# Optimization experiments

Measured on AMD Instinct MI355X. Metric: run time of the kernel, lower is better.

Reference implementation:

```python
import jax, jax.numpy as jnp
import numpy as np

EPS = 1e-6  # torch F.normalize eps


def setup_inputs() -> dict:
    key = jax.random.key(0)
    ks = jax.random.split(key, 9)
    B, C, H, W = 2, 256, 64, 64
    nH, dk, dv = 4, 64, 64
    s = 0.05  # weight scale for numerical stability
    return {
        "x": jax.random.normal(ks[0], (B, C, H, W), jnp.float32),
        "Wq": jax.random.normal(ks[1], (nH, dk, C), jnp.float32) * s,
        "bq": jax.random.normal(ks[2], (nH, dk), jnp.float32) * s,
        "Wk": jax.random.normal(ks[3], (nH, dk, C), jnp.float32) * s,
        "bk": jax.random.normal(ks[4], (nH, dk), jnp.float32) * s,
        "Wv": jax.random.normal(ks[5], (nH, dv, C), jnp.float32) * s,
        "bv": jax.random.normal(ks[6], (nH, dv), jnp.float32) * s,
        "Wm": jax.random.normal(ks[7], (C, nH * dv), jnp.float32) * s,
        "bm": jax.random.normal(ks[8], (C,), jnp.float32) * s,
    }


def _l2norm(t):
    # torch F.normalize along channel dim (axis=2 here: [B,H,dk,L])
    n = jnp.sqrt(jnp.sum(t * t, axis=2, keepdims=True))
    return t / jnp.maximum(n, EPS)


def reference(x, Wq, bq, Wk, bk, Wv, bv, Wm, bm):
    B, C, H, W = x.shape
    nH = Wq.shape[0]
    L = H * W
    xf = x.reshape(B, C, L)  # 1x1 conv == channel matmul on flattened spatial
    # per-head projections: [B, nH, d, L]
    Q = jnp.einsum('bcl,hdc->bhdl', xf, Wq) + bq[None, :, :, None]
    K = jnp.einsum('bcl,hdc->bhdl', xf, Wk) + bk[None, :, :, None]
    V = jnp.einsum('bcl,hvc->bhvl', xf, Wv) + bv[None, :, :, None]
    Q = _l2norm(Q)
    K = _l2norm(K)
    # cosine-similarity scores A[b,h,i,j] = sum_d Q[b,h,d,i] K[b,h,d,j]
    A = jnp.einsum('bhdi,bhdj->bhij', Q, K)
    A = jax.nn.softmax(A, axis=-1)
    # R[b,h,v,i] = sum_j A[b,h,i,j] V[b,h,v,j]
    R = jnp.einsum('bhij,bhvj->bhvi', A, V)
    # concat heads along channels -> [B, nH*dv, L]
    Rc = R.reshape(B, nH * V.shape[2], L)
    out = jnp.einsum('bcl,oc->bol', Rc, Wm) + bm[None, :, None]
    out = out.reshape(B, C, H, W) + x  # residual
    return out
```

## Files before the change

### kernel.cpp

```cpp
#include <hip/hip_runtime.h>
#include <hip/hip_bf16.h>
#include <cstdint>
#include <cstddef>

typedef __bf16 bf16;
typedef bf16 bf16x8 __attribute__((ext_vector_type(8)));
typedef bf16 bf16x4 __attribute__((ext_vector_type(4)));
typedef bf16 bf16x2 __attribute__((ext_vector_type(2)));
typedef float f32x4 __attribute__((ext_vector_type(4)));

#define MFMA16(A, B, Cc) __builtin_amdgcn_mfma_f32_16x16x32_bf16((A), (B), (Cc), 0, 0, 0)
#define GLD16(g, l)                                                          \
  __builtin_amdgcn_global_load_lds(                                          \
      (const __attribute__((address_space(1))) void*)(g),                    \
      (__attribute__((address_space(3))) void*)(l), 16, 0, 0)

static constexpr int L   = 4096;
static constexpr int CH  = 256;
static constexpr int NH  = 4;

static constexpr size_t OFF_WALL = 0;
static constexpr size_t OFF_WMB  = 393216;
static constexpr size_t OFF_BALL = 524288;
static constexpr size_t OFF_XT   = 528384;
static constexpr size_t OFF_QT   = 4722688;
static constexpr size_t OFF_KT   = 8916992;
static constexpr size_t OFF_VD   = 13111296;
static constexpr size_t OFF_RP1  = 17305600;
static constexpr size_t OFF_RP2  = 21499904;
static constexpr size_t OFF_RP3  = 25694208;
static constexpr size_t OFF_DP4  = 29888512;
static constexpr size_t OFF_DP2  = 21499904;
static constexpr size_t NEED4    = 30412800;

__global__ __launch_bounds__(256) void k_wcvt(
    const float* __restrict__ Wq, const float* __restrict__ Wk,
    const float* __restrict__ Wv, const float* __restrict__ bq,
    const float* __restrict__ bk, const float* __restrict__ bv,
    const float* __restrict__ Wm, bf16* __restrict__ Wall,
    float* __restrict__ ball, bf16* __restrict__ Wmb) {
  int id = blockIdx.x * 256 + threadIdx.x;
  if (id < 65536)        Wall[id] = (bf16)Wq[id];
  else if (id < 131072)  Wall[id] = (bf16)Wk[id - 65536];
  else if (id < 196608)  Wall[id] = (bf16)Wv[id - 131072];
  else if (id < 262144)  Wmb[id - 196608] = (bf16)Wm[id - 196608];
  else if (id < 262912) {
    int k = id - 262144;
    ball[k] = (k < 256) ? bq[k] : (k < 512) ? bk[k - 256] : bv[k - 512];
  }
}

__global__ __launch_bounds__(256) void k_tx(const float* __restrict__ x,
                                            bf16* __restrict__ xT) {
  __shared__ float t[32][33];
  const int b = blockIdx.z, c0 = blockIdx.y * 32, l0 = blockIdx.x * 32;
  const int tx = threadIdx.x, ty = threadIdx.y;
  #pragma unroll
  for (int i = 0; i < 4; ++i) {
    int c = c0 + ty + 8 * i;
    t[ty + 8 * i][tx] = x[((size_t)b * CH + c) * L + l0 + tx];
  }
  __syncthreads();
  #pragma unroll
  for (int i = 0; i < 4; ++i) {
    int l = l0 + ty + 8 * i;
    xT[((size_t)b * L + l) * CH + c0 + tx] = (bf16)t[tx][ty + 8 * i];
  }
}

__global__ __launch_bounds__(256) void k_proj(
    const bf16* __restrict__ Wall, const float* __restrict__ ball,
    const bf16* __restrict__ xT, bf16* __restrict__ Qt,
    bf16* __restrict__ Kt, bf16* __restrict__ Vd) {
  const int b = blockIdx.z, strip = blockIdx.y, lt = blockIdx.x;
  const int w = threadIdx.x >> 6;
  const int lane = threadIdx.x & 63;
  const int lo = lane & 15, g = lane >> 4;
  const int l0 = lt * 256 + w * 64;

  const bf16* wbase = Wall + (size_t)strip * 64 * CH;
  const bf16* xbase = xT + (size_t)b * L * CH;

  f32x4 acc[4][4];
  #pragma unroll
  for (int m = 0; m < 4; ++m)
    #pragma unroll
    for (int n = 0; n < 4; ++n) acc[m][n] = (f32x4){0.f, 0.f, 0.f, 0.f};

  #pragma unroll
  for (int kc = 0; kc < 8; ++kc) {
    bf16x8 aw[4], bx[4];
    #pragma unroll
    for (int m = 0; m < 4; ++m)
      aw[m] = *(const bf16x8*)(wbase + (size_t)(16 * m + lo) * CH + kc * 32 + g * 8);
    #pragma unroll
    for (int n = 0; n < 4; ++n)
      bx[n] = *(const bf16x8*)(xbase + (size_t)(l0 + 16 * n + lo) * CH + kc * 32 + g * 8);
    #pragma unroll
    for (int m = 0; m < 4; ++m)
      #pragma unroll
      for (int n = 0; n < 4; ++n) acc[m][n] = MFMA16(aw[m], bx[n], acc[m][n]);
  }

  #pragma unroll
  for (int m = 0; m < 4; ++m)
    #pragma unroll
    for (int r = 0; r < 4; ++r) {
      float bias = ball[strip * 64 + 16 * m + 4 * g + r];
      #pragma unroll
      for (int n = 0; n < 4; ++n) acc[m][n][r] += bias;
    }

  if (strip < 8) {
    #pragma unroll
    for (int n = 0; n < 4; ++n) {
      float ss = 0.f;
      #pragma unroll
      for (int m = 0; m < 4; ++m)
        #pragma unroll
        for (int r = 0; r < 4; ++r) ss += acc[m][n][r] * acc[m][n][r];
      ss += __shfl_xor(ss, 16);
      ss += __shfl_xor(ss, 32);
      float sc = 1.f / fmaxf(sqrtf(ss), 1e-6f);
      #pragma unroll
      for (int m = 0; m < 4; ++m)
        #pragma unroll
        for (int r = 0; r < 4; ++r) acc[m][n][r] *= sc;
    }
    bf16* dst = (strip < 4) ? Qt : Kt;
    const int h = strip & 3;
    #pragma unroll
    for (int n = 0; n < 4; ++n) {
      const int l = l0 + 16 * n + lo;
      #pragma unroll
      for (int m = 0; m < 4; ++m) {
        size_t base = ((size_t)(b * NH + h) * L + l) * 64 + 16 * m + 4 * g;
        bf16x2 v01, v23;
        v01[0] = (bf16)acc[m][n][0]; v01[1] = (bf16)acc[m][n][1];
        v23[0] = (bf16)acc[m][n][2]; v23[1] = (bf16)acc[m][n][3];
        *(bf16x2*)(dst + base)     = v01;
        *(bf16x2*)(dst + base + 2) = v23;
      }
    }
  } else {
    const int h = strip - 8;
    #pragma unroll
    for (int m = 0; m < 4; ++m)
      #pragma unroll
      for (int r = 0; r < 4; ++r) {
        const int d = 16 * m + 4 * g + r;
        #pragma unroll
        for (int n = 0; n < 4; ++n) {
          const int l = l0 + 16 * n + lo;
          Vd[((size_t)(b * NH + h) * 64 + d) * L + l] = (bf16)acc[m][n][r];
        }
      }
  }
}


#define STAGE(bb, j0)                                                          \
  {                                                                            \
    const char* gk0 = kbase + (size_t)((j0) + sr) * 128 + scS;                 \
    const char* gk1 = kbase + (size_t)((j0) + 32 + sr) * 128 + scS;            \
    const char* gv0 = vbase + (size_t)sr * 8192 + (size_t)(j0) * 2 + scS;      \
    const char* gv1 = vbase + (size_t)(32 + sr) * 8192 + (size_t)(j0) * 2 + scS; \
    GLD16(gk0, kbuf[bb] + w * 1024 + lane * 16);                               \
    GLD16(gk1, kbuf[bb] + 4096 + w * 1024 + lane * 16);                        \
    GLD16(gv0, vbuf[bb] + w * 1024 + lane * 16);                               \
    GLD16(gv1, vbuf[bb] + 4096 + w * 1024 + lane * 16);                        \
  }

#define COMPUTE(bb)                                                            \
  {                                                                            \
    const char* kb = kbuf[bb];                                                 \
    const char* vb = vbuf[bb];                                                 \
    _Pragma("unroll") for (int t = 0; t < 4; ++t) {                            \
      bf16x8 kf0 = *(const bf16x8*)(kb + (16 * t + lo) * 128 + ((16 * g) ^ sw)); \
      bf16x8 kf1 = *(const bf16x8*)(kb + (16 * t + lo) * 128 + ((64 + 16 * g) ^ sw)); \
      _Pragma("unroll") for (int m = 0; m < 4; ++m) {                          \
        f32x4 z = (f32x4){0.f, 0.f, 0.f, 0.f};                                 \
        z = MFMA16(kf0, qf[m][0], z);                                          \
        z = MFMA16(kf1, qf[m][1], z);                                          \
        float p0 = __expf(z[0]), p1 = __expf(z[1]);                            \
        float p2 = __expf(z[2]), p3 = __expf(z[3]);                            \
        den[m] += (p0 + p1) + (p2 + p3);                                       \
        bf16x4 pk;                                                             \
        pk[0] = (bf16)p0; pk[1] = (bf16)p1; pk[2] = (bf16)p2; pk[3] = (bf16)p3; \
        *(bf16x4*)(pbw + (16 * m + lo) * 128 + ((32 * t + 8 * g) ^ sw)) = pk;  \
      }                                                                        \
    }                                                                          \
    bf16x8 pa[4][2];                                                           \
    _Pragma("unroll") for (int m = 0; m < 4; ++m)                              \
      _Pragma("unroll") for (int s = 0; s < 2; ++s)                            \
        pa[m][s] = *(const bf16x8*)(pbw + (16 * m + lo) * 128 + ((64 * s + 16 * g) ^ sw)); \
    _Pragma("unroll") for (int n = 0; n < 4; ++n) {                            \
      bf16x8 vf0 = *(const bf16x8*)(vb + (16 * n + lo) * 128 + ((16 * g) ^ sw)); \
      bf16x8 vf1 = *(const bf16x8*)(vb + (16 * n + lo) * 128 + ((64 + 16 * g) ^ sw)); \
      _Pragma("unroll") for (int m = 0; m < 4; ++m) {                          \
        racc[m][n] = MFMA16(pa[m][0], vf0, racc[m][n]);                        \
        racc[m][n] = MFMA16(pa[m][1], vf1, racc[m][n]);                        \
      }                                                                        \
    }                                                                          \
  }

template <int JS>
__global__ __launch_bounds__(256, 2) void k_attn(
    const bf16* __restrict__ Qt, const bf16* __restrict__ Kt,
    const bf16* __restrict__ Vd, bf16* __restrict__ R0,
    bf16* __restrict__ R1, bf16* __restrict__ R2, bf16* __restrict__ R3,
    float* __restrict__ D0, float* __restrict__ D1,
    float* __restrict__ D2, float* __restrict__ D3) {
  const int id = blockIdx.x;
  const int bh = id & 7;
  const int qt = (id >> 3) & 15;
  const int js = id >> 7;
  const int tid = threadIdx.x;
  const int w = tid >> 6;
  const int lane = tid & 63;
  const int lo = lane & 15, g = lane >> 4;
  const int sw = (lo & 7) << 4;
  const int i0 = qt * 256 + w * 64;

  __shared__ __align__(16) char kbuf[2][8192];
  __shared__ __align__(16) char vbuf[2][8192];
  __shared__ __align__(16) char pbuf[4][8192];
  char* pbw = pbuf[w];

  const char* kbase = (const char*)(Kt + (size_t)bh * L * 64);
  const char* vbase = (const char*)(Vd + (size_t)bh * 64 * L);

  const int sr = tid >> 3;
  const int sc = (tid & 7) * 16;
  const int scS = sc ^ ((sr & 7) << 4);

  const bf16* qb = Qt + ((size_t)bh * L + i0) * 64;
  bf16x8 qf[4][2];
  #pragma unroll
  for (int m = 0; m < 4; ++m)
    #pragma unroll
    for (int s = 0; s < 2; ++s)
      qf[m][s] = *(const bf16x8*)(qb + (size_t)(16 * m + lo) * 64 + 32 * s + 8 * g);

  f32x4 racc[4][4];
  #pragma unroll
  for (int m = 0; m < 4; ++m)
    #pragma unroll
    for (int n = 0; n < 4; ++n) racc[m][n] = (f32x4){0.f, 0.f, 0.f, 0.f};
  float den[4] = {0.f, 0.f, 0.f, 0.f};

  const int jbeg = js * (L / JS);
  const int nt = (L / JS) / 64;

  STAGE(0, jbeg)
  __syncthreads();
  for (int it = 0; it < nt; ++it) {
    const int bb = it & 1;
    if (it + 1 < nt) STAGE(bb ^ 1, jbeg + (it + 1) * 64)
    COMPUTE(bb)
    __syncthreads();
  }

  #pragma unroll
  for (int m = 0; m < 4; ++m) {
    den[m] += __shfl_xor(den[m], 16);
    den[m] += __shfl_xor(den[m], 32);
  }

  bf16* rp = (js == 0) ? R0 : (js == 1) ? R1 : (js == 2) ? R2 : R3;
  float* dp = (js == 0) ? D0 : (js == 1) ? D1 : (js == 2) ? D2 : D3;

  if (g == 0) {
    #pragma unroll
    for (int m = 0; m < 4; ++m)
      dp[(size_t)bh * L + i0 + 16 * m + lo] = den[m];
  }
  #pragma unroll
  for (int m = 0; m < 4; ++m)
    #pragma unroll
    for (int n = 0; n < 4; ++n)
      #pragma unroll
      for (int r = 0; r < 4; ++r) {
        const int q = 16 * m + 4 * g + r;
        rp[((size_t)bh * L + i0 + q) * 64 + 16 * n + lo] = (bf16)racc[m][n][r];
      }
}

template <int JS>
__global__ __launch_bounds__(256) void k_comb(
    const bf16* __restrict__ R0, const bf16* __restrict__ R1,
    const bf16* __restrict__ R2, const bf16* __restrict__ R3,
    const float* __restrict__ D0, const float* __restrict__ D1,
    const float* __restrict__ D2, const float* __restrict__ D3,
    bf16* __restrict__ Rt) {
  const int tid = blockIdx.x * 256 + threadIdx.x;
  const int e8 = tid * 8;
  const int d8 = e8 & 63;
  const int l = (e8 >> 6) & (L - 1);
  const int bh = e8 >> 18;
  const size_t di = (size_t)bh * L + l;
  float den = D0[di] + D1[di];
  if (JS == 4) den += D2[di] + D3[di];
  const float inv = 1.0f / den;
  bf16x8 a0 = *(const bf16x8*)(R0 + e8);
  bf16x8 a1 = *(const bf16x8*)(R1 + e8);
  bf16x8 o;
  if (JS == 4) {
    bf16x8 a2 = *(const bf16x8*)(R2 + e8);
    bf16x8 a3 = *(const bf16x8*)(R3 + e8);
    #pragma unroll
    for (int e = 0; e < 8; ++e)
      o[e] = (bf16)((((float)a0[e] + (float)a1[e]) + ((float)a2[e] + (float)a3[e])) * inv);
  } else {
    #pragma unroll
    for (int e = 0; e < 8; ++e)
      o[e] = (bf16)(((float)a0[e] + (float)a1[e]) * inv);
  }
  *(bf16x8*)(Rt + ((size_t)(bh >> 2) * L + l) * CH + (bh & 3) * 64 + d8) = o;
}

__global__ __launch_bounds__(256) void k_out(
    const bf16* __restrict__ Wmb, const bf16* __restrict__ Rt,
    const float* __restrict__ x, const float* __restrict__ bm,
    float* __restrict__ out) {
  const int b = blockIdx.y, lt = blockIdx.x;
  const int w = threadIdx.x >> 6;
  const int lane = threadIdx.x & 63;
  const int lo = lane & 15, g = lane >> 4;
  const int o0 = w * 64, l0 = lt * 64;

  f32x4 acc[4][4];
  #pragma unroll
  for (int m = 0; m < 4; ++m)
    #pragma unroll
    for (int n = 0; n < 4; ++n) acc[m][n] = (f32x4){0.f, 0.f, 0.f, 0.f};

  #pragma unroll
  for (int kc = 0; kc < 8; ++kc) {
    bf16x8 aw[4], bx[4];
    #pragma unroll
    for (int m = 0; m < 4; ++m)
      aw[m] = *(const bf16x8*)(Wmb + (size_t)(o0 + 16 * m + lo) * CH + kc * 32 + g * 8);
    #pragma unroll
    for (int n = 0; n < 4; ++n)
      bx[n] = *(const bf16x8*)(Rt + ((size_t)b * L + l0 + 16 * n + lo) * CH + kc * 32 + g * 8);
    #pragma unroll
    for (int m = 0; m < 4; ++m)
      #pragma unroll
      for (int n = 0; n < 4; ++n) acc[m][n] = MFMA16(aw[m], bx[n], acc[m][n]);
  }

  #pragma unroll
  for (int m = 0; m < 4; ++m)
    #pragma unroll
    for (int r = 0; r < 4; ++r) {
      const int o = o0 + 16 * m + 4 * g + r;
      const float bias = bm[o];
      #pragma unroll
      for (int n = 0; n < 4; ++n) {
        const int l = l0 + 16 * n + lo;
        size_t idx = ((size_t)b * CH + o) * (size_t)L + l;
        out[idx] = acc[m][n][r] + bias + x[idx];
      }
    }
}

extern "C" void kernel_launch(void* const* d_in, const int* in_sizes, int n_in,
                              void* d_out, int out_size, void* d_ws, size_t ws_size,
                              hipStream_t stream) {
  const float* x  = (const float*)d_in[0];
  const float* Wq = (const float*)d_in[1];
  const float* bq = (const float*)d_in[2];
  const float* Wk = (const float*)d_in[3];
  const float* bk = (const float*)d_in[4];
  const float* Wv = (const float*)d_in[5];
  const float* bv = (const float*)d_in[6];
  const float* Wm = (const float*)d_in[7];
  const float* bm = (const float*)d_in[8];
  float* out = (float*)d_out;

  char* ws = (char*)d_ws;
  bf16*  Wall = (bf16*)(ws + OFF_WALL);
  bf16*  Wmb  = (bf16*)(ws + OFF_WMB);
  float* ball = (float*)(ws + OFF_BALL);
  bf16*  xT   = (bf16*)(ws + OFF_XT);
  bf16*  Qt   = (bf16*)(ws + OFF_QT);
  bf16*  Kt   = (bf16*)(ws + OFF_KT);
  bf16*  Vd   = (bf16*)(ws + OFF_VD);

  bf16* Rp0 = (bf16*)(ws + OFF_XT);
  bf16* Rp1 = (bf16*)(ws + OFF_RP1);
  bf16* Rt  = (bf16*)(ws + OFF_QT);

  k_wcvt<<<1027, 256, 0, stream>>>(Wq, Wk, Wv, bq, bk, bv, Wm, Wall, ball, Wmb);
  k_tx<<<dim3(L / 32, CH / 32, 2), dim3(32, 8), 0, stream>>>(x, xT);
  k_proj<<<dim3(16, 12, 2), 256, 0, stream>>>(Wall, ball, xT, Qt, Kt, Vd);

  if (ws_size >= NEED4) {
    bf16*  Rp2 = (bf16*)(ws + OFF_RP2);
    bf16*  Rp3 = (bf16*)(ws + OFF_RP3);
    float* Dp  = (float*)(ws + OFF_DP4);
    float* D0 = Dp, *D1 = Dp + 32768, *D2 = Dp + 65536, *D3 = Dp + 98304;
    k_attn<4><<<512, 256, 0, stream>>>(Qt, Kt, Vd, Rp0, Rp1, Rp2, Rp3, D0, D1, D2, D3);
    k_comb<4><<<1024, 256, 0, stream>>>(Rp0, Rp1, Rp2, Rp3, D0, D1, D2, D3, Rt);
  } else {
    float* Dp = (float*)(ws + OFF_DP2);
    float* D0 = Dp, *D1 = Dp + 32768;
    k_attn<2><<<256, 256, 0, stream>>>(Qt, Kt, Vd, Rp0, Rp1, nullptr, nullptr, D0, D1, nullptr, nullptr);
    k_comb<2><<<1024, 256, 0, stream>>>(Rp0, Rp1, nullptr, nullptr, D0, D1, nullptr, nullptr, Rt);
  }

  k_out<<<dim3(64, 2), 256, 0, stream>>>(Wmb, Rt, x, bm, out);
}
```

Before: 107.0 us.

## Switch attention to 32x32 MFMA with register-resident P, fuse prep and combine kernels

The attention inner loop now uses 32x32x16 bf16 MFMA, so the softmax probabilities stay in registers and feed the PV MFMA directly. This drops the per-wave LDS P buffer and its write and read round trip. To match the register layout, V columns are permuted when stored in the projection kernel. Separately, the weight-conversion and transpose kernels are merged into one launch, and the split-K combine is folded into the output GEMM, which removes a kernel and the Rt round trip. The cost is higher register pressure from the 16-wide accumulators and a smaller output-GEMM tile that re-reads the partial results.

```diff
diff --git a/kernel.cpp b/kernel.cpp
--- a/kernel.cpp
+++ b/kernel.cpp
@@ -8,8 +8,10 @@
 typedef bf16 bf16x4 __attribute__((ext_vector_type(4)));
 typedef bf16 bf16x2 __attribute__((ext_vector_type(2)));
 typedef float f32x4 __attribute__((ext_vector_type(4)));
+typedef float f32x16 __attribute__((ext_vector_type(16)));
 
 #define MFMA16(A, B, Cc) __builtin_amdgcn_mfma_f32_16x16x32_bf16((A), (B), (Cc), 0, 0, 0)
+#define MFMA32(A, B, Cc) __builtin_amdgcn_mfma_f32_32x32x16_bf16((A), (B), (Cc), 0, 0, 0)
 #define GLD16(g, l)                                                          \
   __builtin_amdgcn_global_load_lds(                                          \
       (const __attribute__((address_space(1))) void*)(g),                    \
@@ -33,38 +35,43 @@
 static constexpr size_t OFF_DP2  = 21499904;
 static constexpr size_t NEED4    = 30412800;
 
-__global__ __launch_bounds__(256) void k_wcvt(
+__global__ __launch_bounds__(256) void k_prep(
     const float* __restrict__ Wq, const float* __restrict__ Wk,
     const float* __restrict__ Wv, const float* __restrict__ bq,
     const float* __restrict__ bk, const float* __restrict__ bv,
-    const float* __restrict__ Wm, bf16* __restrict__ Wall,
-    float* __restrict__ ball, bf16* __restrict__ Wmb) {
-  int id = blockIdx.x * 256 + threadIdx.x;
-  if (id < 65536)        Wall[id] = (bf16)Wq[id];
-  else if (id < 131072)  Wall[id] = (bf16)Wk[id - 65536];
-  else if (id < 196608)  Wall[id] = (bf16)Wv[id - 131072];
-  else if (id < 262144)  Wmb[id - 196608] = (bf16)Wm[id - 196608];
-  else if (id < 262912) {
-    int k = id - 262144;
-    ball[k] = (k < 256) ? bq[k] : (k < 512) ? bk[k - 256] : bv[k - 512];
-  }
-}
-
-__global__ __launch_bounds__(256) void k_tx(const float* __restrict__ x,
-                                            bf16* __restrict__ xT) {
+    const float* __restrict__ Wm, const float* __restrict__ x,
+    bf16* __restrict__ Wall, float* __restrict__ ball,
+    bf16* __restrict__ Wmb, bf16* __restrict__ xT) {
   __shared__ float t[32][33];
-  const int b = blockIdx.z, c0 = blockIdx.y * 32, l0 = blockIdx.x * 32;
-  const int tx = threadIdx.x, ty = threadIdx.y;
-  #pragma unroll
-  for (int i = 0; i < 4; ++i) {
-    int c = c0 + ty + 8 * i;
-    t[ty + 8 * i][tx] = x[((size_t)b * CH + c) * L + l0 + tx];
-  }
-  __syncthreads();
-  #pragma unroll
-  for (int i = 0; i < 4; ++i) {
-    int l = l0 + ty + 8 * i;
-    xT[((size_t)b * L + l) * CH + c0 + tx] = (bf16)t[tx][ty + 8 * i];
+  const int bid = blockIdx.x;
+  const int tid = threadIdx.x;
+  if (bid < 1027) {
+    int id = bid * 256 + tid;
+    if (id < 65536)        Wall[id] = (bf16)Wq[id];
+    else if (id < 131072)  Wall[id] = (bf16)Wk[id - 65536];
+    else if (id < 196608)  Wall[id] = (bf16)Wv[id - 131072];
+    else if (id < 262144)  Wmb[id - 196608] = (bf16)Wm[id - 196608];
+    else if (id < 262912) {
+      int k = id - 262144;
+      ball[k] = (k < 256) ? bq[k] : (k < 512) ? bk[k - 256] : bv[k - 512];
+    }
+  } else {
+    const int id = bid - 1027;
+    const int b = id >> 10;
+    const int c0 = ((id >> 7) & 7) * 32;
+    const int l0 = (id & 127) * 32;
+    const int tx = tid & 31, ty = tid >> 5;
+    #pragma unroll
+    for (int i = 0; i < 4; ++i) {
+      int c = c0 + ty + 8 * i;
+      t[ty + 8 * i][tx] = x[((size_t)b * CH + c) * L + l0 + tx];
+    }
+    __syncthreads();
+    #pragma unroll
+    for (int i = 0; i < 4; ++i) {
+      int l = l0 + ty + 8 * i;
+      xT[((size_t)b * L + l) * CH + c0 + tx] = (bf16)t[tx][ty + 8 * i];
+    }
   }
 }
 
@@ -144,6 +151,7 @@
     }
   } else {
     const int h = strip - 8;
+    const int lop = (lo & 3) | ((lo & 4) << 1) | ((lo & 8) >> 1);
     #pragma unroll
     for (int m = 0; m < 4; ++m)
       #pragma unroll
@@ -151,7 +159,7 @@
         const int d = 16 * m + 4 * g + r;
         #pragma unroll
         for (int n = 0; n < 4; ++n) {
-          const int l = l0 + 16 * n + lo;
+          const int l = l0 + 16 * n + lop;
           Vd[((size_t)(b * NH + h) * 64 + d) * L + l] = (bf16)acc[m][n][r];
         }
       }
@@ -165,41 +173,46 @@
     const char* gk1 = kbase + (size_t)((j0) + 32 + sr) * 128 + scS;            \
     const char* gv0 = vbase + (size_t)sr * 8192 + (size_t)(j0) * 2 + scS;      \
     const char* gv1 = vbase + (size_t)(32 + sr) * 8192 + (size_t)(j0) * 2 + scS; \
-    GLD16(gk0, kbuf[bb] + w * 1024 + lane * 16);                               \
-    GLD16(gk1, kbuf[bb] + 4096 + w * 1024 + lane * 16);                        \
-    GLD16(gv0, vbuf[bb] + w * 1024 + lane * 16);                               \
-    GLD16(gv1, vbuf[bb] + 4096 + w * 1024 + lane * 16);                        \
+    GLD16(gk0, kbuf[bb] + tid * 16);                                           \
+    GLD16(gk1, kbuf[bb] + 4096 + tid * 16);                                    \
+    GLD16(gv0, vbuf[bb] + tid * 16);                                           \
+    GLD16(gv1, vbuf[bb] + 4096 + tid * 16);                                    \
   }
 
 #define COMPUTE(bb)                                                            \
   {                                                                            \
     const char* kb = kbuf[bb];                                                 \
     const char* vb = vbuf[bb];                                                 \
-    _Pragma("unroll") for (int t = 0; t < 4; ++t) {                            \
-      bf16x8 kf0 = *(const bf16x8*)(kb + (16 * t + lo) * 128 + ((16 * g) ^ sw)); \
-      bf16x8 kf1 = *(const bf16x8*)(kb + (16 * t + lo) * 128 + ((64 + 16 * g) ^ sw)); \
-      _Pragma("unroll") for (int m = 0; m < 4; ++m) {                          \
-        f32x4 z = (f32x4){0.f, 0.f, 0.f, 0.f};                                 \
-        z = MFMA16(kf0, qf[m][0], z);                                          \
-        z = MFMA16(kf1, qf[m][1], z);                                          \
-        float p0 = __expf(z[0]), p1 = __expf(z[1]);                            \
-        float p2 = __expf(z[2]), p3 = __expf(z[3]);                            \
-        den[m] += (p0 + p1) + (p2 + p3);                                       \
-        bf16x4 pk;                                                             \
-        pk[0] = (bf16)p0; pk[1] = (bf16)p1; pk[2] = (bf16)p2; pk[3] = (bf16)p3; \
-        *(bf16x4*)(pbw + (16 * m + lo) * 128 + ((32 * t + 8 * g) ^ sw)) = pk;  \
-      }                                                                        \
-    }                                                                          \
-    bf16x8 pa[4][2];                                                           \
-    _Pragma("unroll") for (int m = 0; m < 4; ++m)                              \
-      _Pragma("unroll") for (int s = 0; s < 2; ++s)                            \
-        pa[m][s] = *(const bf16x8*)(pbw + (16 * m + lo) * 128 + ((64 * s + 16 * g) ^ sw)); \
-    _Pragma("unroll") for (int n = 0; n < 4; ++n) {                            \
-      bf16x8 vf0 = *(const bf16x8*)(vb + (16 * n + lo) * 128 + ((16 * g) ^ sw)); \
-      bf16x8 vf1 = *(const bf16x8*)(vb + (16 * n + lo) * 128 + ((64 + 16 * g) ^ sw)); \
-      _Pragma("unroll") for (int m = 0; m < 4; ++m) {                          \
-        racc[m][n] = MFMA16(pa[m][0], vf0, racc[m][n]);                        \
-        racc[m][n] = MFMA16(pa[m][1], vf1, racc[m][n]);                        \
+    _Pragma("unroll") for (int jb = 0; jb < 2; ++jb) {                         \
+      bf16x8 kf[4], vf[2][2];                                                  \
+      _Pragma("unroll") for (int f = 0; f < 4; ++f)                            \
+        kf[f] = *(const bf16x8*)(kb + (32 * jb + ln) * 128 +                   \
+                                 ((32 * f + 16 * hi) ^ sw));                   \
+      _Pragma("unroll") for (int dvb = 0; dvb < 2; ++dvb)                      \
+        _Pragma("unroll") for (int c = 0; c < 2; ++c)                          \
+          vf[dvb][c] = *(const bf16x8*)(vb + (32 * dvb + ln) * 128 +           \
+                                        ((64 * jb + 32 * c + 16 * hi) ^ sw));  \
+      _Pragma("unroll") for (int qb = 0; qb < 2; ++qb) {                       \
+        f32x16 z;                                                              \
+        _Pragma("unroll") for (int r = 0; r < 16; ++r) z[r] = 0.f;             \
+        _Pragma("unroll") for (int f = 0; f < 4; ++f)                          \
+          z = MFMA32(kf[f], qf[qb][f], z);                                     \
+        float p[16];                                                           \
+        _Pragma("unroll") for (int r = 0; r < 16; ++r) p[r] = __expf(z[r]);    \
+        float t0 = (p[0] + p[1]) + (p[2] + p[3]);                              \
+        float t1 = (p[4] + p[5]) + (p[6] + p[7]);                              \
+        float t2 = (p[8] + p[9]) + (p[10] + p[11]);                            \
+        float t3 = (p[12] + p[13]) + (p[14] + p[15]);                          \
+        den[qb] += (t0 + t1) + (t2 + t3);                                      \
+        bf16x8 pf0, pf1;                                                       \
+        _Pragma("unroll") for (int e = 0; e < 8; ++e) {                        \
+          pf0[e] = (bf16)p[e];                                                 \
+          pf1[e] = (bf16)p[8 + e];                                             \
+        }                                                                      \
+        _Pragma("unroll") for (int dvb = 0; dvb < 2; ++dvb) {                  \
+          racc[qb][dvb] = MFMA32(pf0, vf[dvb][0], racc[qb][dvb]);              \
+          racc[qb][dvb] = MFMA32(pf1, vf[dvb][1], racc[qb][dvb]);              \
+        }                                                                      \
       }                                                                        \
     }                                                                          \
   }
@@ -218,14 +231,12 @@
   const int tid = threadIdx.x;
   const int w = tid >> 6;
   const int lane = tid & 63;
-  const int lo = lane & 15, g = lane >> 4;
-  const int sw = (lo & 7) << 4;
+  const int ln = lane & 31, hi = lane >> 5;
+  const int sw = (ln & 7) << 4;
   const int i0 = qt * 256 + w * 64;
 
   __shared__ __align__(16) char kbuf[2][8192];
   __shared__ __align__(16) char vbuf[2][8192];
-  __shared__ __align__(16) char pbuf[4][8192];
-  char* pbw = pbuf[w];
 
   const char* kbase = (const char*)(Kt + (size_t)bh * L * 64);
   const char* vbase = (const char*)(Vd + (size_t)bh * 64 * L);
@@ -234,20 +245,22 @@
   const int sc = (tid & 7) * 16;
   const int scS = sc ^ ((sr & 7) << 4);
 
-  const bf16* qb = Qt + ((size_t)bh * L + i0) * 64;
-  bf16x8 qf[4][2];
-  #pragma unroll
-  for (int m = 0; m < 4; ++m)
-    #pragma unroll
-    for (int s = 0; s < 2; ++s)
-      qf[m][s] = *(const bf16x8*)(qb + (size_t)(16 * m + lo) * 64 + 32 * s + 8 * g);
-
-  f32x4 racc[4][4];
-  #pragma unroll
-  for (int m = 0; m < 4; ++m)
-    #pragma unroll
-    for (int n = 0; n < 4; ++n) racc[m][n] = (f32x4){0.f, 0.f, 0.f, 0.f};
-  float den[4] = {0.f, 0.f, 0.f, 0.f};
+  const bf16* qbp = Qt + ((size_t)bh * L + i0) * 64;
+  bf16x8 qf[2][4];
+  #pragma unroll
+  for (int qb = 0; qb < 2; ++qb)
+    #pragma unroll
+    for (int f = 0; f < 4; ++f)
+      qf[qb][f] = *(const bf16x8*)(qbp + (size_t)(32 * qb + ln) * 64 + 16 * f + 8 * hi);
+
+  f32x16 racc[2][2];
+  #pragma unroll
+  for (int qb = 0; qb < 2; ++qb)
+    #pragma unroll
+    for (int dvb = 0; dvb < 2; ++dvb)
+      #pragma unroll
+      for (int r = 0; r < 16; ++r) racc[qb][dvb][r] = 0.f;
+  float den[2] = {0.f, 0.f};
 
   const int jbeg = js * (L / JS);
   const int nt = (L / JS) / 64;
@@ -262,92 +275,92 @@
   }
 
   #pragma unroll
-  for (int m = 0; m < 4; ++m) {
-    den[m] += __shfl_xor(den[m], 16);
-    den[m] += __shfl_xor(den[m], 32);
-  }
+  for (int qb = 0; qb < 2; ++qb) den[qb] += __shfl_xor(den[qb], 32);
 
   bf16* rp = (js == 0) ? R0 : (js == 1) ? R1 : (js == 2) ? R2 : R3;
   float* dp = (js == 0) ? D0 : (js == 1) ? D1 : (js == 2) ? D2 : D3;
 
-  if (g == 0) {
-    #pragma unroll
-    for (int m = 0; m < 4; ++m)
-      dp[(size_t)bh * L + i0 + 16 * m + lo] = den[m];
-  }
-  #pragma unroll
-  for (int m = 0; m < 4; ++m)
-    #pragma unroll
-    for (int n = 0; n < 4; ++n)
-      #pragma unroll
-      for (int r = 0; r < 4; ++r) {
-        const int q = 16 * m + 4 * g + r;
-        rp[((size_t)bh * L + i0 + q) * 64 + 16 * n + lo] = (bf16)racc[m][n][r];
+  if (hi == 0) {
+    #pragma unroll
+    for (int qb = 0; qb < 2; ++qb)
+      dp[(size_t)bh * L + i0 + 32 * qb + ln] = den[qb];
+  }
+  #pragma unroll
+  for (int qb = 0; qb < 2; ++qb)
+    #pragma unroll
+    for (int dvb = 0; dvb < 2; ++dvb)
+      #pragma unroll
+      for (int r = 0; r < 16; ++r) {
+        const int q = 32 * qb + (r & 3) + 8 * (r >> 2) + 4 * hi;
+        rp[((size_t)bh * L + i0 + q) * 64 + 32 * dvb + ln] = (bf16)racc[qb][dvb][r];
       }
 }
 
 template <int JS>
-__global__ __launch_bounds__(256) void k_comb(
-    const bf16* __restrict__ R0, const bf16* __restrict__ R1,
-    const bf16* __restrict__ R2, const bf16* __restrict__ R3,
-    const float* __restrict__ D0, const float* __restrict__ D1,
-    const float* __restrict__ D2, const float* __restrict__ D3,
-    bf16* __restrict__ Rt) {
-  const int tid = blockIdx.x * 256 + threadIdx.x;
-  const int e8 = tid * 8;
-  const int d8 = e8 & 63;
-  const int l = (e8 >> 6) & (L - 1);
-  const int bh = e8 >> 18;
-  const size_t di = (size_t)bh * L + l;
-  float den = D0[di] + D1[di];
-  if (JS == 4) den += D2[di] + D3[di];
-  const float inv = 1.0f / den;
-  bf16x8 a0 = *(const bf16x8*)(R0 + e8);
-  bf16x8 a1 = *(const bf16x8*)(R1 + e8);
-  bf16x8 o;
-  if (JS == 4) {
-    bf16x8 a2 = *(const bf16x8*)(R2 + e8);
-    bf16x8 a3 = *(const bf16x8*)(R3 + e8);
-    #pragma unroll
-    for (int e = 0; e < 8; ++e)
-      o[e] = (bf16)((((float)a0[e] + (float)a1[e]) + ((float)a2[e] + (float)a3[e])) * inv);
-  } else {
-    #pragma unroll
-    for (int e = 0; e < 8; ++e)
-      o[e] = (bf16)(((float)a0[e] + (float)a1[e]) * inv);
-  }
-  *(bf16x8*)(Rt + ((size_t)(bh >> 2) * L + l) * CH + (bh & 3) * 64 + d8) = o;
-}
-
 __global__ __launch_bounds__(256) void k_out(
-    const bf16* __restrict__ Wmb, const bf16* __restrict__ Rt,
-    const float* __restrict__ x, const float* __restrict__ bm,
-    float* __restrict__ out) {
+    const bf16* __restrict__ Wmb, const bf16* __restrict__ R0,
+    const bf16* __restrict__ R1, const bf16* __restrict__ R2,
+    const bf16* __restrict__ R3, const float* __restrict__ D0,
+    const float* __restrict__ D1, const float* __restrict__ D2,
+    const float* __restrict__ D3, const float* __restrict__ x,
+    const float* __restrict__ bm, float* __restrict__ out) {
   const int b = blockIdx.y, lt = blockIdx.x;
   const int w = threadIdx.x >> 6;
   const int lane = threadIdx.x & 63;
   const int lo = lane & 15, g = lane >> 4;
-  const int o0 = w * 64, l0 = lt * 64;
-
-  f32x4 acc[4][4];
+  const int o0 = w * 64, l0 = lt * 32;
+
+  float invd[2][4];
+  #pragma unroll
+  for (int n = 0; n < 2; ++n) {
+    const int l = l0 + 16 * n + lo;
+    #pragma unroll
+    for (int h = 0; h < 4; ++h) {
+      const size_t di = (size_t)(b * NH + h) * L + l;
+      float dd = D0[di] + D1[di];
+      if (JS == 4) dd += D2[di] + D3[di];
+      invd[n][h] = 1.0f / dd;
+    }
+  }
+
+  f32x4 acc[4][2];
   #pragma unroll
   for (int m = 0; m < 4; ++m)
     #pragma unroll
-    for (int n = 0; n < 4; ++n) acc[m][n] = (f32x4){0.f, 0.f, 0.f, 0.f};
+    for (int n = 0; n < 2; ++n) acc[m][n] = (f32x4){0.f, 0.f, 0.f, 0.f};
 
   #pragma unroll
   for (int kc = 0; kc < 8; ++kc) {
-    bf16x8 aw[4], bx[4];
+    bf16x8 aw[4], bx[2];
     #pragma unroll
     for (int m = 0; m < 4; ++m)
       aw[m] = *(const bf16x8*)(Wmb + (size_t)(o0 + 16 * m + lo) * CH + kc * 32 + g * 8);
-    #pragma unroll
-    for (int n = 0; n < 4; ++n)
-      bx[n] = *(const bf16x8*)(Rt + ((size_t)b * L + l0 + 16 * n + lo) * CH + kc * 32 + g * 8);
+    const int h = kc >> 1;
+    #pragma unroll
+    for (int n = 0; n < 2; ++n) {
+      const size_t base = ((size_t)(b * NH + h) * L + (l0 + 16 * n + lo)) * 64 +
+                          (kc & 1) * 32 + 8 * g;
+      bf16x8 r0 = *(const bf16x8*)(R0 + base);
+      bf16x8 r1 = *(const bf16x8*)(R1 + base);
+      const float iv = invd[n][h];
+      if (JS == 4) {
+        bf16x8 r2 = *(const bf16x8*)(R2 + base);
+        bf16x8 r3 = *(const bf16x8*)(R3 + base);
+        #pragma unroll
+        for (int e = 0; e < 8; ++e) {
+          float s = ((float)r0[e] + (float)r1[e]) + ((float)r2[e] + (float)r3[e]);
+          bx[n][e] = (bf16)(s * iv);
+        }
+      } else {
+        #pragma unroll
+        for (int e = 0; e < 8; ++e)
+          bx[n][e] = (bf16)(((float)r0[e] + (float)r1[e]) * iv);
+      }
+    }
     #pragma unroll
     for (int m = 0; m < 4; ++m)
       #pragma unroll
-      for (int n = 0; n < 4; ++n) acc[m][n] = MFMA16(aw[m], bx[n], acc[m][n]);
+      for (int n = 0; n < 2; ++n) acc[m][n] = MFMA16(aw[m], bx[n], acc[m][n]);
   }
 
   #pragma unroll
@@ -357,7 +370,7 @@
       const int o = o0 + 16 * m + 4 * g + r;
       const float bias = bm[o];
       #pragma unroll
-      for (int n = 0; n < 4; ++n) {
+      for (int n = 0; n < 2; ++n) {
         const int l = l0 + 16 * n + lo;
         size_t idx = ((size_t)b * CH + o) * (size_t)L + l;
         out[idx] = acc[m][n][r] + bias + x[idx];
@@ -390,10 +403,8 @@
 
   bf16* Rp0 = (bf16*)(ws + OFF_XT);
   bf16* Rp1 = (bf16*)(ws + OFF_RP1);
-  bf16* Rt  = (bf16*)(ws + OFF_QT);
-
-  k_wcvt<<<1027, 256, 0, stream>>>(Wq, Wk, Wv, bq, bk, bv, Wm, Wall, ball, Wmb);
-  k_tx<<<dim3(L / 32, CH / 32, 2), dim3(32, 8), 0, stream>>>(x, xT);
+
+  k_prep<<<3075, 256, 0, stream>>>(Wq, Wk, Wv, bq, bk, bv, Wm, x, Wall, ball, Wmb, xT);
   k_proj<<<dim3(16, 12, 2), 256, 0, stream>>>(Wall, ball, xT, Qt, Kt, Vd);
 
   if (ws_size >= NEED4) {
@@ -402,13 +413,14 @@
     float* Dp  = (float*)(ws + OFF_DP4);
     float* D0 = Dp, *D1 = Dp + 32768, *D2 = Dp + 65536, *D3 = Dp + 98304;
     k_attn<4><<<512, 256, 0, stream>>>(Qt, Kt, Vd, Rp0, Rp1, Rp2, Rp3, D0, D1, D2, D3);
-    k_comb<4><<<1024, 256, 0, stream>>>(Rp0, Rp1, Rp2, Rp3, D0, D1, D2, D3, Rt);
+    k_out<4><<<dim3(128, 2), 256, 0, stream>>>(Wmb, Rp0, Rp1, Rp2, Rp3, D0, D1, D2, D3,
+                                               x, bm, out);
   } else {
     float* Dp = (float*)(ws + OFF_DP2);
     float* D0 = Dp, *D1 = Dp + 32768;
-    k_attn<2><<<256, 256, 0, stream>>>(Qt, Kt, Vd, Rp0, Rp1, nullptr, nullptr, D0, D1, nullptr, nullptr);
-    k_comb<2><<<1024, 256, 0, stream>>>(Rp0, Rp1, nullptr, nullptr, D0, D1, nullptr, nullptr, Rt);
-  }
-
-  k_out<<<dim3(64, 2), 256, 0, stream>>>(Wmb, Rt, x, bm, out);
+    k_attn<2><<<256, 256, 0, stream>>>(Qt, Kt, Vd, Rp0, Rp1, nullptr, nullptr,
+                                       D0, D1, nullptr, nullptr);
+    k_out<2><<<dim3(128, 2), 256, 0, stream>>>(Wmb, Rp0, Rp1, nullptr, nullptr,
+                                               D0, D1, nullptr, nullptr, x, bm, out);
+  }
 }
```

Result: faster. 90.94 us, median of 2 (-15.0%).
